# Kernel tuning notes

Measured on AMD Instinct MI355X. Metric: run time of the kernel, lower is better.

Reference implementation:

```python
import jax, jax.numpy as jnp
import numpy as np

N_NODES = 100000


def gcn_conv(x, edge_index, W, b, n_nodes):
    # GCNConv: out = D^{-1/2} (A + I) D^{-1/2} X W + b  (add_self_loops=True)
    xw = x @ W  # [N, F_out]
    loop = jnp.arange(n_nodes, dtype=edge_index.dtype)
    row = jnp.concatenate([edge_index[0], loop])  # source
    col = jnp.concatenate([edge_index[1], loop])  # target
    ones = jnp.ones(row.shape[0], dtype=x.dtype)
    deg = jax.ops.segment_sum(ones, col, num_segments=n_nodes)
    dinv = jnp.where(deg > 0, jax.lax.rsqrt(deg), 0.0)
    norm = dinv[row] * dinv[col]  # [E+N]
    msgs = norm[:, None] * xw[row]  # gather + scale
    out = jax.ops.segment_sum(msgs, col, num_segments=n_nodes)  # scatter-add
    return out + b


def setup_inputs() -> dict:
    key = jax.random.key(0)
    k1, k2, k3, k4 = jax.random.split(key, 4)
    x = jax.random.normal(k1, (N_NODES, 512), dtype=jnp.float32)
    edge_index = jax.random.randint(k2, (2, 3200000), 0, N_NODES, dtype=jnp.int64)
    W1 = jax.random.normal(k3, (512, 16), dtype=jnp.float32) * (1.0 / np.sqrt(512))
    b1 = jnp.zeros((16,), dtype=jnp.float32)
    W2 = jax.random.normal(k4, (16, 7), dtype=jnp.float32) * (1.0 / np.sqrt(16))
    b2 = jnp.zeros((7,), dtype=jnp.float32)
    return {"x": x, "edge_index": edge_index, "W1": W1, "b1": b1, "W2": W2, "b2": b2}


def reference(x, edge_index, W1, b1, W2, b2):
    n = x.shape[0]
    h = gcn_conv(x, edge_index, W1, b1, n)
    h = jax.nn.relu(h)
    # F.dropout(training=self.training) is identity in eval mode
    h = gcn_conv(h, edge_index, W2, b2, n)
    return jax.nn.log_softmax(h, axis=1)
```

## Files before the change

### kernel.cpp

```cpp
#include <hip/hip_runtime.h>
#include <math.h>
#include <stdint.h>

#define NBMAX 1024
#define BCAP 4864

typedef __attribute__((ext_vector_type(8))) short short8;
typedef __attribute__((ext_vector_type(4))) float f32x4;

__device__ __forceinline__ unsigned int f2bf(float f) {
    unsigned int u = __float_as_uint(f);
    return (u + 0x7FFFu + ((u >> 16) & 1u)) >> 16;
}
__device__ __forceinline__ float bl(unsigned int u) { return __uint_as_float(u << 16); }
__device__ __forceinline__ float bh(unsigned int u) { return __uint_as_float(u & 0xFFFF0000u); }

__global__ void k_init(int* __restrict__ cursor) {
    int i = blockIdx.x * 512 + threadIdx.x;
    if (i < NBMAX) cursor[i] = i * BCAP;
}

__global__ __launch_bounds__(256) void k_gemm(
    const float* __restrict__ x, const float* __restrict__ W1,
    float* __restrict__ xw, int n) {
    __shared__ struct { uint4 bhi[1024]; uint4 blo[1024]; } sh;
    for (int s = threadIdx.x; s < 1024; s += 256) {
        int ts = s >> 6, l = s & 63;
        int colc = l & 15, kg2 = l >> 4;
        int kbase = ts * 32 + kg2 * 8;
        unsigned int hw[8], lw[8];
#pragma unroll
        for (int j = 0; j < 8; ++j) {
            float wv = W1[(size_t)(kbase + j) * 16 + colc];
            unsigned int u = __float_as_uint(wv);
            unsigned int h = u >> 16;
            unsigned int lo = f2bf(wv - bl(h));
            hw[j] = h; lw[j] = lo;
        }
        uint4 ph, pl;
        ph.x = hw[0] | (hw[1] << 16); ph.y = hw[2] | (hw[3] << 16);
        ph.z = hw[4] | (hw[5] << 16); ph.w = hw[6] | (hw[7] << 16);
        pl.x = lw[0] | (lw[1] << 16); pl.y = lw[2] | (lw[3] << 16);
        pl.z = lw[4] | (lw[5] << 16); pl.w = lw[6] | (lw[7] << 16);
        sh.bhi[s] = ph; sh.blo[s] = pl;
    }
    __syncthreads();

    int w = threadIdx.x >> 6, lane = threadIdx.x & 63;
    int mtMax = (n + 15) >> 4;
    int mt = blockIdx.x * 4 + w;
    if (mt >= mtMax) return;
    int rowbase = mt * 16;
    int r0 = rowbase + (lane & 15);
    if (r0 >= n) r0 = n - 1;
    int kg = lane >> 4;
    const float4* xr = (const float4*)(x + (size_t)r0 * 512);
    f32x4 acc = {0.f, 0.f, 0.f, 0.f};
#pragma unroll 2
    for (int ts = 0; ts < 16; ++ts) {
        float4 u = xr[ts * 8 + kg * 2];
        float4 v = xr[ts * 8 + kg * 2 + 1];
        float e[8] = {u.x, u.y, u.z, u.w, v.x, v.y, v.z, v.w};
        short8 ah, al;
#pragma unroll
        for (int j = 0; j < 8; ++j) {
            unsigned int uu = __float_as_uint(e[j]);
            unsigned int h = uu >> 16;
            unsigned int lo = f2bf(e[j] - bl(h));
            ah[j] = (short)h;
            al[j] = (short)lo;
        }
        uint4 bhw = sh.bhi[ts * 64 + lane];
        uint4 blw = sh.blo[ts * 64 + lane];
        short8 bhv = *reinterpret_cast<const short8*>(&bhw);
        short8 blv = *reinterpret_cast<const short8*>(&blw);
        acc = __builtin_amdgcn_mfma_f32_16x16x32_bf16(ah, bhv, acc, 0, 0, 0);
        acc = __builtin_amdgcn_mfma_f32_16x16x32_bf16(al, bhv, acc, 0, 0, 0);
        acc = __builtin_amdgcn_mfma_f32_16x16x32_bf16(ah, blv, acc, 0, 0, 0);
    }
#pragma unroll
    for (int r = 0; r < 4; ++r) {
        int orow = rowbase + kg * 4 + r;
        if (orow < n) xw[(size_t)orow * 16 + (lane & 15)] = acc[r];
    }
}

__global__ __launch_bounds__(512) void k_bucket(
    const int* __restrict__ row, const int* __restrict__ col,
    int* __restrict__ cursor, unsigned int* __restrict__ sortedG, int E) {
    __shared__ int histL[NBMAX];
    __shared__ int offsL[NBMAX];
    __shared__ int gbL[NBMAX];
    __shared__ int sbuf[NBMAX];
    __shared__ unsigned int stageW[4096];
    __shared__ unsigned short stageB[4096];
    int t = threadIdx.x;
    for (int i = t; i < NBMAX; i += 512) histL[i] = 0;
    __syncthreads();
    int off = blockIdx.x * 4096;
    unsigned int w[8]; int bk[8]; int rk[8];
#pragma unroll
    for (int i = 0; i < 8; ++i) {
        int e = off + t + i * 512;
        if (e < E) {
            int c = col[e], r = row[e];
            w[i]  = ((unsigned int)r << 7) | (unsigned int)(c & 127);
            bk[i] = c >> 7;
            rk[i] = atomicAdd(&histL[bk[i]], 1);
        } else bk[i] = -1;
    }
    __syncthreads();
    sbuf[t] = histL[t];
    sbuf[t + 512] = histL[t + 512];
    __syncthreads();
    for (int o = 1; o < NBMAX; o <<= 1) {
        int v0 = (t >= o) ? sbuf[t - o] : 0;
        int v1 = (t + 512 >= o) ? sbuf[t + 512 - o] : 0;
        __syncthreads();
        sbuf[t] += v0;
        sbuf[t + 512] += v1;
        __syncthreads();
    }
    for (int s = t; s < NBMAX; s += 512) {
        int cnt = histL[s];
        offsL[s] = sbuf[s] - cnt;
        gbL[s]   = cnt ? atomicAdd(&cursor[s], cnt) : 0;
    }
    __syncthreads();
#pragma unroll
    for (int i = 0; i < 8; ++i) {
        if (bk[i] >= 0) {
            int s2 = offsL[bk[i]] + rk[i];
            stageW[s2] = w[i];
            stageB[s2] = (unsigned short)bk[i];
        }
    }
    __syncthreads();
    int total = min(4096, E - off);
    for (int s2 = t; s2 < total; s2 += 512) {
        int b = stageB[s2];
        sortedG[gbL[b] + (s2 - offsL[b])] = stageW[s2];
    }
}

__global__ __launch_bounds__(512) void k_sortscale(
    unsigned int* __restrict__ sortedG, const int* __restrict__ cursor,
    int2* __restrict__ offsE, float* __restrict__ dinv,
    const float* __restrict__ xw, unsigned int* __restrict__ sxwh, int N) {
    __shared__ unsigned int wv[BCAP];
    __shared__ int hist[128];
    __shared__ int off_[128];
    __shared__ int sc[128];
    __shared__ float ds[128];
    int t = threadIdx.x, b = blockIdx.x;
    if (t < 128) hist[t] = 0;
    __syncthreads();
    int beg = b * BCAP;
    int cnt = cursor[b] - beg;
    for (int i = t; i < cnt; i += 512) {
        unsigned int w = sortedG[beg + i];
        wv[i] = w;
        atomicAdd(&hist[w & 127], 1);
    }
    __syncthreads();
    if (t < 128) sc[t] = hist[t];
    __syncthreads();
    for (int o = 1; o < 128; o <<= 1) {
        int v = 0;
        if (t < 128 && t >= o) v = sc[t - o];
        __syncthreads();
        if (t < 128) sc[t] += v;
        __syncthreads();
    }
    if (t < 128) {
        int d = hist[t];
        off_[t] = sc[t] - d;
        int node = b * 128 + t;
        float dv = rsqrtf((float)(d + 1));
        ds[t] = dv;
        if (node < N) {
            int pos = beg + off_[t];
            offsE[node] = make_int2(pos, pos + d);
            dinv[node] = dv;
        }
        hist[t] = 0;
    }
    __syncthreads();
    for (int i = t; i < cnt; i += 512) {
        unsigned int w = wv[i];
        int c = w & 127;
        int r2 = atomicAdd(&hist[c], 1);
        sortedG[beg + off_[c] + r2] = w >> 7;
    }
    const float4* xw4 = (const float4*)xw;
    uint2* dsth = (uint2*)sxwh;
    int nl = t >> 2;
    int node = b * 128 + nl;
    if (node < N) {
        float s = ds[nl];
        float4 v = xw4[(size_t)b * 512 + t];
        unsigned int u0 = f2bf(v.x * s), u1 = f2bf(v.y * s);
        unsigned int u2 = f2bf(v.z * s), u3 = f2bf(v.w * s);
        uint2 o; o.x = u0 | (u1 << 16); o.y = u2 | (u3 << 16);
        dsth[(size_t)b * 512 + t] = o;
    }
}

__global__ __launch_bounds__(256) void k_gather1f(
    const int2* __restrict__ offsE, const int* __restrict__ srow,
    const uint4* __restrict__ s4, const float* __restrict__ dinv,
    const float* __restrict__ W2, const float* __restrict__ b1,
    float* __restrict__ sxw2p, int N) {
    __shared__ float sW2[112];
    __shared__ float sb1[16];
    if (threadIdx.x < 112) sW2[threadIdx.x] = W2[threadIdx.x];
    if (threadIdx.x < 16) sb1[threadIdx.x] = b1[threadIdx.x];
    __syncthreads();
    int idx = blockIdx.x * 256 + threadIdx.x;
    int node = idx >> 2, sub = idx & 3;
    int q = sub & 1, seg = sub >> 1;
    if (node >= N) return;
    int2 oe = offsE[node];
    int beg0 = oe.x, end0 = oe.y;
    int mid = beg0 + ((end0 - beg0) >> 1);
    int beg = seg ? mid : beg0;
    int end = seg ? end0 : mid;

    float a0 = 0.f, a1 = 0.f, a2 = 0.f, a3 = 0.f;
    float a4 = 0.f, a5 = 0.f, a6 = 0.f, a7 = 0.f;
    if (seg == 0) {
        uint4 sv = s4[(size_t)node * 2 + q];
        a0 = bl(sv.x); a1 = bh(sv.x); a2 = bl(sv.y); a3 = bh(sv.y);
        a4 = bl(sv.z); a5 = bh(sv.z); a6 = bl(sv.w); a7 = bh(sv.w);
    }
    int j = beg;
    for (; j + 3 < end; j += 4) {
        int r0 = srow[j], r1 = srow[j + 1], r2 = srow[j + 2], r3 = srow[j + 3];
        uint4 v0 = s4[(size_t)r0 * 2 + q];
        uint4 v1 = s4[(size_t)r1 * 2 + q];
        uint4 v2 = s4[(size_t)r2 * 2 + q];
        uint4 v3 = s4[(size_t)r3 * 2 + q];
        a0 += (bl(v0.x) + bl(v1.x)) + (bl(v2.x) + bl(v3.x));
        a1 += (bh(v0.x) + bh(v1.x)) + (bh(v2.x) + bh(v3.x));
        a2 += (bl(v0.y) + bl(v1.y)) + (bl(v2.y) + bl(v3.y));
        a3 += (bh(v0.y) + bh(v1.y)) + (bh(v2.y) + bh(v3.y));
        a4 += (bl(v0.z) + bl(v1.z)) + (bl(v2.z) + bl(v3.z));
        a5 += (bh(v0.z) + bh(v1.z)) + (bh(v2.z) + bh(v3.z));
        a6 += (bl(v0.w) + bl(v1.w)) + (bl(v2.w) + bl(v3.w));
        a7 += (bh(v0.w) + bh(v1.w)) + (bh(v2.w) + bh(v3.w));
    }
    for (; j < end; ++j) {
        int r = srow[j];
        uint4 v = s4[(size_t)r * 2 + q];
        a0 += bl(v.x); a1 += bh(v.x); a2 += bl(v.y); a3 += bh(v.y);
        a4 += bl(v.z); a5 += bh(v.z); a6 += bl(v.w); a7 += bh(v.w);
    }
    a0 += __shfl_xor(a0, 2, 64); a1 += __shfl_xor(a1, 2, 64);
    a2 += __shfl_xor(a2, 2, 64); a3 += __shfl_xor(a3, 2, 64);
    a4 += __shfl_xor(a4, 2, 64); a5 += __shfl_xor(a5, 2, 64);
    a6 += __shfl_xor(a6, 2, 64); a7 += __shfl_xor(a7, 2, 64);
    float d = dinv[node];
    float h[8];
    h[0] = fmaxf(fmaf(d, a0, sb1[q * 8 + 0]), 0.f);
    h[1] = fmaxf(fmaf(d, a1, sb1[q * 8 + 1]), 0.f);
    h[2] = fmaxf(fmaf(d, a2, sb1[q * 8 + 2]), 0.f);
    h[3] = fmaxf(fmaf(d, a3, sb1[q * 8 + 3]), 0.f);
    h[4] = fmaxf(fmaf(d, a4, sb1[q * 8 + 4]), 0.f);
    h[5] = fmaxf(fmaf(d, a5, sb1[q * 8 + 5]), 0.f);
    h[6] = fmaxf(fmaf(d, a6, sb1[q * 8 + 6]), 0.f);
    h[7] = fmaxf(fmaf(d, a7, sb1[q * 8 + 7]), 0.f);
    float o[7] = {0.f, 0.f, 0.f, 0.f, 0.f, 0.f, 0.f};
    int rbase = q * 8;
#pragma unroll
    for (int i = 0; i < 8; ++i) {
        float hv = h[i];
#pragma unroll
        for (int jj = 0; jj < 7; ++jj) o[jj] = fmaf(hv, sW2[(rbase + i) * 7 + jj], o[jj]);
    }
#pragma unroll
    for (int jj = 0; jj < 7; ++jj) o[jj] += __shfl_xor(o[jj], 1, 64);
    if (seg == 0) {
        float4 wv4;
        if (q == 0) { wv4.x = o[0] * d; wv4.y = o[1] * d; wv4.z = o[2] * d; wv4.w = o[3] * d; }
        else        { wv4.x = o[4] * d; wv4.y = o[5] * d; wv4.z = o[6] * d; wv4.w = 0.f; }
        ((float4*)sxw2p)[(size_t)node * 2 + q] = wv4;
    }
}

__global__ __launch_bounds__(256) void k_gather2f(
    const int2* __restrict__ offsE, const int* __restrict__ srow,
    const float* __restrict__ sxw2p, const float* __restrict__ dinv,
    const float* __restrict__ b2, float* __restrict__ out, int N) {
    __shared__ float sb2[8];
    if (threadIdx.x < 7) sb2[threadIdx.x] = b2[threadIdx.x];
    if (threadIdx.x == 7) sb2[7] = 0.f;
    __syncthreads();
    int idx = blockIdx.x * 256 + threadIdx.x;
    int node = idx >> 2, sub = idx & 3;
    int q = sub & 1, seg = sub >> 1;
    if (node >= N) return;
    int2 oe = offsE[node];
    int beg0 = oe.x, end0 = oe.y;
    int mid = beg0 + ((end0 - beg0) >> 1);
    int beg = seg ? mid : beg0;
    int end = seg ? end0 : mid;
    const float4* s4 = (const float4*)sxw2p;
    float4 a = {0.f, 0.f, 0.f, 0.f};
    if (seg == 0) a = s4[(size_t)node * 2 + q];
    int j = beg;
    for (; j + 3 < end; j += 4) {
        int r0 = srow[j], r1 = srow[j + 1], r2 = srow[j + 2], r3 = srow[j + 3];
        float4 v0 = s4[(size_t)r0 * 2 + q];
        float4 v1 = s4[(size_t)r1 * 2 + q];
        float4 v2 = s4[(size_t)r2 * 2 + q];
        float4 v3 = s4[(size_t)r3 * 2 + q];
        a.x += (v0.x + v1.x) + (v2.x + v3.x);
        a.y += (v0.y + v1.y) + (v2.y + v3.y);
        a.z += (v0.z + v1.z) + (v2.z + v3.z);
        a.w += (v0.w + v1.w) + (v2.w + v3.w);
    }
    for (; j < end; ++j) {
        int r = srow[j];
        float4 v = s4[(size_t)r * 2 + q];
        a.x += v.x; a.y += v.y; a.z += v.z; a.w += v.w;
    }
    a.x += __shfl_xor(a.x, 2, 64); a.y += __shfl_xor(a.y, 2, 64);
    a.z += __shfl_xor(a.z, 2, 64); a.w += __shfl_xor(a.w, 2, 64);
    float d = dinv[node];
    float z0 = fmaf(d, a.x, sb2[q * 4 + 0]);
    float z1 = fmaf(d, a.y, sb2[q * 4 + 1]);
    float z2 = fmaf(d, a.z, sb2[q * 4 + 2]);
    float z3 = (q == 0) ? fmaf(d, a.w, sb2[3]) : -INFINITY;
    float m = fmaxf(fmaxf(z0, z1), fmaxf(z2, z3));
    m = fmaxf(m, __shfl_xor(m, 1, 64));
    float s = expf(z0 - m) + expf(z1 - m) + expf(z2 - m) + ((q == 0) ? expf(z3 - m) : 0.f);
    s += __shfl_xor(s, 1, 64);
    float l = m + logf(s);
    if (seg == 0) {
        float* ob = out + (size_t)node * 7;
        if (q == 0) { ob[0] = z0 - l; ob[1] = z1 - l; ob[2] = z2 - l; ob[3] = z3 - l; }
        else        { ob[4] = z0 - l; ob[5] = z1 - l; ob[6] = z2 - l; }
    }
}

extern "C" void kernel_launch(void* const* d_in, const int* in_sizes, int n_in,
                              void* d_out, int out_size, void* d_ws, size_t ws_size,
                              hipStream_t stream) {
    const float* x  = (const float*)d_in[0];
    const int*   ei = (const int*)d_in[1];
    const float* W1 = (const float*)d_in[2];
    const float* b1 = (const float*)d_in[3];
    const float* W2 = (const float*)d_in[4];
    const float* b2 = (const float*)d_in[5];

    int N = in_sizes[0] / 512;
    int E = in_sizes[1] / 2;
    const int* row = ei;
    const int* col = ei + E;

    int NB = (N + 127) >> 7;

    int* cursor = (int*)d_ws;
    int2* offsE = (int2*)(cursor + NBMAX);
    float* dinv = (float*)(offsE + N);
    unsigned int* sortedG = (unsigned int*)(dinv + N);
    float* xw1  = (float*)(sortedG + (size_t)NBMAX * BCAP);
    unsigned int* sxwh = (unsigned int*)(xw1 + (size_t)16 * N);
    float* sxw2p = xw1;
    float* out   = (float*)d_out;

    int mtMax = (N + 15) / 16;
    int gM = (mtMax + 3) / 4;
    int bB = (E + 4095) / 4096;
    int gP = (4 * N + 255) / 256;

    k_init     <<<2, 512, 0, stream>>>(cursor);
    k_gemm     <<<gM, 256, 0, stream>>>(x, W1, xw1, N);
    k_bucket   <<<bB, 512, 0, stream>>>(row, col, cursor, sortedG, E);
    k_sortscale<<<NB, 512, 0, stream>>>(sortedG, cursor, offsE, dinv, xw1, sxwh, N);
    k_gather1f <<<gP, 256, 0, stream>>>(offsE, (const int*)sortedG, (const uint4*)sxwh,
                                        dinv, W2, b1, sxw2p, N);
    k_gather2f <<<gP, 256, 0, stream>>>(offsE, (const int*)sortedG, sxw2p, dinv, b2, out, N);
}
```

Before: 414.4 us.

## Merge GEMM and edge bucketing into one kernel with interleaved block roles

Fuses the dense x@W1 MFMA kernel and the edge bucketing kernel into a single launch. Even blocks do bucketing and odd blocks do the GEMM, with shared memory unioned between the two roles. The goal is to overlap the bandwidth-heavy GEMM read of x with the atomic- and scatter-heavy bucketing, and to remove one launch and its serialization. GEMM blocks grow to 512 threads (8 waves). The union takes the larger of the two shared-memory footprints, which may lower occupancy for GEMM blocks.

```diff
diff --git a/kernel.cpp b/kernel.cpp
--- a/kernel.cpp
+++ b/kernel.cpp
@@ -20,11 +20,73 @@
     if (i < NBMAX) cursor[i] = i * BCAP;
 }
 
-__global__ __launch_bounds__(256) void k_gemm(
+__global__ __launch_bounds__(512) void k_bg(
+    const int* __restrict__ row, const int* __restrict__ col,
+    int* __restrict__ cursor, unsigned int* __restrict__ sortedG, int E, int bB,
     const float* __restrict__ x, const float* __restrict__ W1,
     float* __restrict__ xw, int n) {
-    __shared__ struct { uint4 bhi[1024]; uint4 blo[1024]; } sh;
-    for (int s = threadIdx.x; s < 1024; s += 256) {
+    __shared__ union {
+        struct {
+            int histL[NBMAX]; int offsL[NBMAX]; int gbL[NBMAX]; int sbuf[NBMAX];
+            unsigned int stageW[4096]; unsigned short stageB[4096];
+        } b;
+        struct { uint4 bhi[1024]; uint4 blo[1024]; } g;
+    } sh;
+    int t = threadIdx.x;
+    int pair = blockIdx.x >> 1;
+
+    if ((blockIdx.x & 1) == 0) {
+        if (pair >= bB) return;
+        for (int i = t; i < NBMAX; i += 512) sh.b.histL[i] = 0;
+        __syncthreads();
+        int off = pair * 4096;
+        unsigned int w[8]; int bk[8]; int rk[8];
+#pragma unroll
+        for (int i = 0; i < 8; ++i) {
+            int e = off + t + i * 512;
+            if (e < E) {
+                int c = col[e], r = row[e];
+                w[i]  = ((unsigned int)r << 7) | (unsigned int)(c & 127);
+                bk[i] = c >> 7;
+                rk[i] = atomicAdd(&sh.b.histL[bk[i]], 1);
+            } else bk[i] = -1;
+        }
+        __syncthreads();
+        sh.b.sbuf[t] = sh.b.histL[t];
+        sh.b.sbuf[t + 512] = sh.b.histL[t + 512];
+        __syncthreads();
+        for (int o = 1; o < NBMAX; o <<= 1) {
+            int v0 = (t >= o) ? sh.b.sbuf[t - o] : 0;
+            int v1 = (t + 512 >= o) ? sh.b.sbuf[t + 512 - o] : 0;
+            __syncthreads();
+            sh.b.sbuf[t] += v0;
+            sh.b.sbuf[t + 512] += v1;
+            __syncthreads();
+        }
+        for (int s = t; s < NBMAX; s += 512) {
+            int cnt = sh.b.histL[s];
+            sh.b.offsL[s] = sh.b.sbuf[s] - cnt;
+            sh.b.gbL[s]   = cnt ? atomicAdd(&cursor[s], cnt) : 0;
+        }
+        __syncthreads();
+#pragma unroll
+        for (int i = 0; i < 8; ++i) {
+            if (bk[i] >= 0) {
+                int s2 = sh.b.offsL[bk[i]] + rk[i];
+                sh.b.stageW[s2] = w[i];
+                sh.b.stageB[s2] = (unsigned short)bk[i];
+            }
+        }
+        __syncthreads();
+        int total = min(4096, E - off);
+        for (int s2 = t; s2 < total; s2 += 512) {
+            int b = sh.b.stageB[s2];
+            sortedG[sh.b.gbL[b] + (s2 - sh.b.offsL[b])] = sh.b.stageW[s2];
+        }
+        return;
+    }
+
+    for (int s = t; s < 1024; s += 512) {
         int ts = s >> 6, l = s & 63;
         int colc = l & 15, kg2 = l >> 4;
         int kbase = ts * 32 + kg2 * 8;
@@ -42,13 +104,13 @@
         ph.z = hw[4] | (hw[5] << 16); ph.w = hw[6] | (hw[7] << 16);
         pl.x = lw[0] | (lw[1] << 16); pl.y = lw[2] | (lw[3] << 16);
         pl.z = lw[4] | (lw[5] << 16); pl.w = lw[6] | (lw[7] << 16);
-        sh.bhi[s] = ph; sh.blo[s] = pl;
-    }
-    __syncthreads();
-
-    int w = threadIdx.x >> 6, lane = threadIdx.x & 63;
+        sh.g.bhi[s] = ph; sh.g.blo[s] = pl;
+    }
+    __syncthreads();
+
+    int w = t >> 6, lane = t & 63;
     int mtMax = (n + 15) >> 4;
-    int mt = blockIdx.x * 4 + w;
+    int mt = pair * 8 + w;
     if (mt >= mtMax) return;
     int rowbase = mt * 16;
     int r0 = rowbase + (lane & 15);
@@ -70,8 +132,8 @@
             ah[j] = (short)h;
             al[j] = (short)lo;
         }
-        uint4 bhw = sh.bhi[ts * 64 + lane];
-        uint4 blw = sh.blo[ts * 64 + lane];
+        uint4 bhw = sh.g.bhi[ts * 64 + lane];
+        uint4 blw = sh.g.blo[ts * 64 + lane];
         short8 bhv = *reinterpret_cast<const short8*>(&bhw);
         short8 blv = *reinterpret_cast<const short8*>(&blw);
         acc = __builtin_amdgcn_mfma_f32_16x16x32_bf16(ah, bhv, acc, 0, 0, 0);
@@ -82,64 +144,6 @@
     for (int r = 0; r < 4; ++r) {
         int orow = rowbase + kg * 4 + r;
         if (orow < n) xw[(size_t)orow * 16 + (lane & 15)] = acc[r];
-    }
-}
-
-__global__ __launch_bounds__(512) void k_bucket(
-    const int* __restrict__ row, const int* __restrict__ col,
-    int* __restrict__ cursor, unsigned int* __restrict__ sortedG, int E) {
-    __shared__ int histL[NBMAX];
-    __shared__ int offsL[NBMAX];
-    __shared__ int gbL[NBMAX];
-    __shared__ int sbuf[NBMAX];
-    __shared__ unsigned int stageW[4096];
-    __shared__ unsigned short stageB[4096];
-    int t = threadIdx.x;
-    for (int i = t; i < NBMAX; i += 512) histL[i] = 0;
-    __syncthreads();
-    int off = blockIdx.x * 4096;
-    unsigned int w[8]; int bk[8]; int rk[8];
-#pragma unroll
-    for (int i = 0; i < 8; ++i) {
-        int e = off + t + i * 512;
-        if (e < E) {
-            int c = col[e], r = row[e];
-            w[i]  = ((unsigned int)r << 7) | (unsigned int)(c & 127);
-            bk[i] = c >> 7;
-            rk[i] = atomicAdd(&histL[bk[i]], 1);
-        } else bk[i] = -1;
-    }
-    __syncthreads();
-    sbuf[t] = histL[t];
-    sbuf[t + 512] = histL[t + 512];
-    __syncthreads();
-    for (int o = 1; o < NBMAX; o <<= 1) {
-        int v0 = (t >= o) ? sbuf[t - o] : 0;
-        int v1 = (t + 512 >= o) ? sbuf[t + 512 - o] : 0;
-        __syncthreads();
-        sbuf[t] += v0;
-        sbuf[t + 512] += v1;
-        __syncthreads();
-    }
-    for (int s = t; s < NBMAX; s += 512) {
-        int cnt = histL[s];
-        offsL[s] = sbuf[s] - cnt;
-        gbL[s]   = cnt ? atomicAdd(&cursor[s], cnt) : 0;
-    }
-    __syncthreads();
-#pragma unroll
-    for (int i = 0; i < 8; ++i) {
-        if (bk[i] >= 0) {
-            int s2 = offsL[bk[i]] + rk[i];
-            stageW[s2] = w[i];
-            stageB[s2] = (unsigned short)bk[i];
-        }
-    }
-    __syncthreads();
-    int total = min(4096, E - off);
-    for (int s2 = t; s2 < total; s2 += 512) {
-        int b = stageB[s2];
-        sortedG[gbL[b] + (s2 - offsL[b])] = stageW[s2];
     }
 }
 
@@ -370,13 +374,14 @@
     float* out   = (float*)d_out;
 
     int mtMax = (N + 15) / 16;
-    int gM = (mtMax + 3) / 4;
-    int bB = (E + 4095) / 4096;
+    int gM8 = (mtMax + 7) / 8;
+    int bB  = (E + 4095) / 4096;
+    int nPair = (bB > gM8) ? bB : gM8;
     int gP = (4 * N + 255) / 256;
 
     k_init     <<<2, 512, 0, stream>>>(cursor);
-    k_gemm     <<<gM, 256, 0, stream>>>(x, W1, xw1, N);
-    k_bucket   <<<bB, 512, 0, stream>>>(row, col, cursor, sortedG, E);
+    k_bg       <<<2 * nPair, 512, 0, stream>>>(row, col, cursor, sortedG, E, bB,
+                                               x, W1, xw1, N);
     k_sortscale<<<NB, 512, 0, stream>>>(sortedG, cursor, offsE, dinv, xw1, sxwh, N);
     k_gather1f <<<gP, 256, 0, stream>>>(offsE, (const int*)sortedG, (const uint4*)sxwh,
                                         dinv, W2, b1, sxw2p, N);
```

New measurement: 395.9 us. -4.5%, faster.
